# Kernel tuning notes

Hardware: AMD Instinct MI355X
Metric: run time of the kernel (lower is better)

Reference implementation:

```python
import jax, jax.numpy as jnp
import numpy as np
import math

N_HEADS = 32
N_KV_HEADS = 8
HEAD_DIM = 64
THETA = 10000.0
NEG_INF = -1e9


def _rope_cos_sin(seq_len, dim, dtype=jnp.float32):
    # freqs over even indices, matching torch.arange(0, dim, 2)/dim
    freqs = 1.0 / (THETA ** (jnp.arange(0, dim, 2, dtype=jnp.float32) / dim))  # [dim/2]
    angles = jnp.arange(seq_len, dtype=jnp.float32)[:, None] * freqs[None, :]  # [S, dim/2]
    return jnp.cos(angles).astype(dtype), jnp.sin(angles).astype(dtype)


def _apply_rope(x, cos, sin):
    # x: [B, S, H, D]; pairs (x[...,2i], x[...,2i+1]) rotated as complex numbers
    xr = x[..., 0::2]
    xi = x[..., 1::2]
    # broadcast cos/sin [S, D/2] -> [1, S, 1, D/2]
    c = cos[None, :, None, :]
    s = sin[None, :, None, :]
    or_ = xr * c - xi * s
    oi_ = xr * s + xi * c
    # interleave back: [..., D/2, 2] -> [..., D]
    return jnp.stack([or_, oi_], axis=-1).reshape(x.shape)


def setup_inputs() -> dict:
    key = jax.random.key(0)
    ks = jax.random.split(key, 5)
    B, S, D = 2, 2048, 2048
    KV_D = N_KV_HEADS * HEAD_DIM
    x = jax.random.normal(ks[0], (B, S, D), dtype=jnp.float32)
    sc = 1.0 / math.sqrt(D)
    wq = jax.random.normal(ks[1], (D, D), dtype=jnp.float32) * sc
    wk = jax.random.normal(ks[2], (D, KV_D), dtype=jnp.float32) * sc
    wv = jax.random.normal(ks[3], (D, KV_D), dtype=jnp.float32) * sc
    wo = jax.random.normal(ks[4], (D, D), dtype=jnp.float32) * sc
    # additive causal mask [1, 1, S, S]
    causal = jnp.tril(jnp.ones((S, S), dtype=bool))
    mask = jnp.where(causal, 0.0, NEG_INF).astype(jnp.float32)[None, None]
    return {"x": x, "mask": mask, "wq": wq, "wk": wk, "wv": wv, "wo": wo}


def reference(x, mask, wq, wk, wv, wo):
    B, S, D = x.shape
    n_rep = N_HEADS // N_KV_HEADS
    q = (x @ wq).reshape(B, S, N_HEADS, HEAD_DIM)
    k = (x @ wk).reshape(B, S, N_KV_HEADS, HEAD_DIM)
    v = (x @ wv).reshape(B, S, N_KV_HEADS, HEAD_DIM)
    cos, sin = _rope_cos_sin(S, HEAD_DIM)
    q = _apply_rope(q, cos, sin)
    k = _apply_rope(k, cos, sin)
    # GQA: repeat_interleave kv heads along head dim
    k = jnp.repeat(k, n_rep, axis=2)  # [B, S, H, D]
    v = jnp.repeat(v, n_rep, axis=2)
    scores = jnp.einsum("bqhd,bkhd->bhqk", q, k) / math.sqrt(HEAD_DIM)
    scores = scores + mask
    probs = jax.nn.softmax(scores.astype(jnp.float32), axis=-1).astype(q.dtype)
    out = jnp.einsum("bhqk,bkhd->bqhd", probs, v).reshape(B, S, N_HEADS * HEAD_DIM)
    return out @ wo
```

## Files before the change

kernel.cpp:

```cpp
#include <hip/hip_runtime.h>
#include <hip/hip_bf16.h>


#define S_LEN 2048
#define BATCH 2
#define D_MODEL 2048
#define NH 32
#define NKV 8
#define HD 64
#define KV_D (NKV * HD)
#define QKV_N (D_MODEL + 2 * KV_D)

typedef __attribute__((ext_vector_type(8))) short short8;
typedef __attribute__((ext_vector_type(4))) float float4v;

typedef __attribute__((address_space(1))) const unsigned int gu32;
typedef __attribute__((address_space(3))) unsigned int lu32;

#if __has_builtin(__builtin_amdgcn_exp2f)
#define PEXP(x) __builtin_amdgcn_exp2f(x)
#else
#define PEXP(x) __expf((x) * 0.69314718f)
#endif
#define QSCALE 0.18033688f

__device__ __forceinline__ float bf2f(unsigned short u) {
    unsigned x = ((unsigned)u) << 16;
    return __builtin_bit_cast(float, x);
}
__device__ __forceinline__ unsigned short f2bf(float f) {
    unsigned u = __builtin_bit_cast(unsigned, f);
    unsigned r = (u + 0x7fffu + ((u >> 16) & 1u)) >> 16;
    return (unsigned short)r;
}
__device__ __forceinline__ unsigned short f2bf_fast(float f) {
    return (unsigned short)((__builtin_bit_cast(unsigned, f) + 0x8000u) >> 16);
}

__global__ void cast_f32_bf16(const float* __restrict__ in,
                              unsigned short* __restrict__ out, long n) {
    long i = ((long)blockIdx.x * 256 + threadIdx.x) * 4;
    if (i + 3 >= n) return;
    const float4v v = *(const float4v*)&in[i];
    unsigned short o[4];
    o[0] = f2bf(v[0]); o[1] = f2bf(v[1]); o[2] = f2bf(v[2]); o[3] = f2bf(v[3]);
    *(__attribute__((ext_vector_type(4))) short*)&out[i] =
        *(__attribute__((ext_vector_type(4))) short*)o;
}

__global__ __launch_bounds__(256) void wtrans(const float* __restrict__ in,
                                              unsigned short* __restrict__ out,
                                              int K, int N) {
    __shared__ unsigned short t[32 * 33];
    const int nb = blockIdx.x * 32, kb = blockIdx.y * 32;
    const int c = threadIdx.x & 31, rr = threadIdx.x >> 5;
#pragma unroll
    for (int it = 0; it < 4; ++it) {
        int r = it * 8 + rr;
        t[c * 33 + r] = f2bf(in[(long)(kb + r) * N + nb + c]);
    }
    __syncthreads();
#pragma unroll
    for (int it = 0; it < 4; ++it) {
        int r = it * 8 + rr;
        out[(long)(nb + r) * K + kb + c] = t[r * 33 + c];
    }
}

template <bool F32OUT>
__global__ __launch_bounds__(256, 4) void gemm_bt(const unsigned short* __restrict__ A,
                                                  const unsigned short* __restrict__ BT,
                                                  void* __restrict__ Cv,
                                                  int M, int N, int K) {
    __shared__ unsigned short As[64 * 64];
    __shared__ unsigned short Bs[128 * 64];
    const int tid = threadIdx.x;
    const int wid = tid >> 6, lane = tid & 63;
    const int l15 = lane & 15, quad = lane >> 4;
    const int wm = (wid >> 1) * 32, wn = (wid & 1) * 64;
    const int row0 = blockIdx.x * 64, col0 = blockIdx.y * 128;

    float4v acc[2][4];
    float4v z;
    z[0] = z[1] = z[2] = z[3] = 0.0f;
    for (int mi = 0; mi < 2; ++mi)
        for (int ni = 0; ni < 4; ++ni) acc[mi][ni] = z;

    const int r_ld = (lane >> 3);
    const int cc_ld = (lane & 7) * 8;

    for (int kb = 0; kb < K; kb += 64) {
        __syncthreads();
#pragma unroll
        for (int c = 0; c < 4; ++c) {
            int chunk = c * 4 + wid;
            int r = chunk * 8 + r_ld;
            __builtin_amdgcn_global_load_lds(
                (gu32*)&BT[(long)(col0 + r) * K + kb + cc_ld],
                (lu32*)&Bs[chunk * 512], 16, 0, 0);
            if (c < 2)
                __builtin_amdgcn_global_load_lds(
                    (gu32*)&A[(long)(row0 + r) * K + kb + cc_ld],
                    (lu32*)&As[chunk * 512], 16, 0, 0);
        }
        __syncthreads();
#pragma unroll
        for (int kk = 0; kk < 64; kk += 32) {
            short8 af[2], bf[4];
#pragma unroll
            for (int i = 0; i < 2; ++i)
                af[i] = *(const short8*)&As[(wm + i * 16 + l15) * 64 + kk + quad * 8];
#pragma unroll
            for (int i = 0; i < 4; ++i)
                bf[i] = *(const short8*)&Bs[(wn + i * 16 + l15) * 64 + kk + quad * 8];
#pragma unroll
            for (int mi = 0; mi < 2; ++mi)
#pragma unroll
                for (int ni = 0; ni < 4; ++ni)
                    acc[mi][ni] = __builtin_amdgcn_mfma_f32_16x16x32_bf16(
                        af[mi], bf[ni], acc[mi][ni], 0, 0, 0);
        }
    }
#pragma unroll
    for (int mi = 0; mi < 2; ++mi)
#pragma unroll
        for (int ni = 0; ni < 4; ++ni)
#pragma unroll
            for (int r = 0; r < 4; ++r) {
                int m = row0 + wm + mi * 16 + quad * 4 + r;
                int n = col0 + wn + ni * 16 + l15;
                if (F32OUT)
                    ((float*)Cv)[(long)m * N + n] = acc[mi][ni][r];
                else
                    ((unsigned short*)Cv)[(long)m * N + n] = f2bf(acc[mi][ni][r]);
            }
}

__global__ __launch_bounds__(256) void rope2(unsigned short* __restrict__ qkv) {
    const int i = threadIdx.x & 31;
    const int row = blockIdx.x * 8 + (threadIdx.x >> 5);
    const int s = row & (S_LEN - 1);
    float freq = __expf(-0.28782313f * (float)i);
    float ang = (float)s * freq;
    float c = cosf(ang), sn = sinf(ang);
    unsigned* p = (unsigned*)qkv + ((long)row * QKV_N + 2 * i) / 2;
#pragma unroll
    for (int head = 0; head < 40; ++head) {
        const float qs = (head < 32) ? QSCALE : 1.0f;
        unsigned v = p[head * 32];
        float xr = bf2f((unsigned short)(v & 0xffff));
        float xi = bf2f((unsigned short)(v >> 16));
        unsigned short lo = f2bf((xr * c - xi * sn) * qs);
        unsigned short hi = f2bf((xr * sn + xi * c) * qs);
        p[head * 32] = (unsigned)lo | ((unsigned)hi << 16);
    }
}

__global__ __launch_bounds__(256) void vtrans(const unsigned short* __restrict__ qkv,
                                              unsigned short* __restrict__ Vt) {
    __shared__ unsigned t[64 * 33];
    const int st = blockIdx.x * 64, kh = blockIdx.y, b = blockIdx.z;
    const int tid = threadIdx.x;
    {
        const int r2 = tid >> 3, dbase = (tid & 7) * 8;
        const unsigned short* src =
            qkv + ((long)(b * S_LEN + st + 2 * r2)) * QKV_N + D_MODEL + KV_D + kh * HD + dbase;
        short8 lo = *(const short8*)src;
        short8 hi = *(const short8*)(src + QKV_N);
#pragma unroll
        for (int j = 0; j < 8; ++j)
            t[(dbase + j) * 33 + r2] =
                (unsigned)(unsigned short)lo[j] | ((unsigned)(unsigned short)hi[j] << 16);
    }
    __syncthreads();
    {
        const int d = tid >> 2, sb = (tid & 3) * 8;
        unsigned short o[16];
#pragma unroll
        for (int jj = 0; jj < 8; ++jj) {
            unsigned v = t[d * 33 + sb + jj];
            o[2 * jj] = (unsigned short)(v & 0xffff);
            o[2 * jj + 1] = (unsigned short)(v >> 16);
        }
        unsigned short* dst =
            Vt + ((long)((b * 8 + kh) * 64 + d)) * S_LEN + st + sb * 2;
        *(short8*)dst = *(short8*)&o[0];
        *(short8*)(dst + 8) = *(short8*)&o[8];
    }
}

__global__ __launch_bounds__(512, 4) void flash4(const unsigned short* __restrict__ qkv,
                                                 const unsigned short* __restrict__ Vt,
                                                 unsigned short* __restrict__ O) {
    __shared__ unsigned short Ks[64 * 72];
    __shared__ unsigned short Vs[64 * 72];
    __shared__ unsigned short Ps[8][16 * 72];

    const int tid = threadIdx.x, w = tid >> 6, lane = tid & 63;
    const int l15 = lane & 15, quad = lane >> 4;
    const int h = blockIdx.y, b = blockIdx.z;
    const int kh = h >> 2, bkh = b * 8 + kh;
    const int qtA = blockIdx.x;

    const int r_st = tid >> 3;
    const int c_st = (tid & 7) * 8;

    float4v z;
    z[0] = z[1] = z[2] = z[3] = 0.0f;

    for (int tsel = 0; tsel < 2; ++tsel) {
        const int qt = tsel ? (15 - qtA) : qtA;
        const int m0 = qt * 128;
        const int row_w = m0 + w * 16;

        short8 aq[2];
        {
            const long qrow = ((long)(b * S_LEN) + row_w + l15) * QKV_N + h * HD;
            aq[0] = *(const short8*)&qkv[qrow + quad * 8];
            aq[1] = *(const short8*)&qkv[qrow + 32 + quad * 8];
        }

        float4v oacc[4];
        float lp[4];
#pragma unroll
        for (int nt = 0; nt < 4; ++nt) oacc[nt] = z;
#pragma unroll
        for (int r = 0; r < 4; ++r) lp[r] = 0.0f;

        const int nkt = 2 * qt + 2;
        for (int kti = 0; kti < nkt; ++kti) {
            const int k0 = kti * 64;
            __syncthreads();
            *(short8*)&Ks[r_st * 72 + c_st] =
                *(const short8*)&qkv[((long)(b * S_LEN) + k0 + r_st) * QKV_N +
                                     D_MODEL + kh * HD + c_st];
            *(short8*)&Vs[r_st * 72 + c_st] =
                *(const short8*)&Vt[((long)bkh * 64 + r_st) * S_LEN + k0 + c_st];
            __syncthreads();

            if (row_w + 15 < k0) continue;

            const bool maskband = (kti >= 2 * qt);

#pragma unroll
            for (int nt = 0; nt < 4; ++nt) {
                short8 bk0 = *(const short8*)&Ks[(nt * 16 + l15) * 72 + quad * 8];
                short8 bk1 = *(const short8*)&Ks[(nt * 16 + l15) * 72 + 32 + quad * 8];
                float4v s = __builtin_amdgcn_mfma_f32_16x16x32_bf16(aq[0], bk0, z, 0, 0, 0);
                s = __builtin_amdgcn_mfma_f32_16x16x32_bf16(aq[1], bk1, s, 0, 0, 0);
#pragma unroll
                for (int r = 0; r < 4; ++r) {
                    const int qidx = row_w + quad * 4 + r;
                    float v = s[r];
                    if (maskband && (k0 + nt * 16 + l15 > qidx)) v = -1e4f;
                    float p = PEXP(v);
                    lp[r] += p;
                    Ps[w][(quad * 4 + r) * 72 + nt * 16 + l15] = f2bf_fast(p);
                }
            }

            short8 ap0 = *(const short8*)&Ps[w][l15 * 72 + quad * 8];
            short8 ap1 = *(const short8*)&Ps[w][l15 * 72 + 32 + quad * 8];
#pragma unroll
            for (int nt = 0; nt < 4; ++nt) {
                short8 bv0 = *(const short8*)&Vs[(nt * 16 + l15) * 72 + quad * 8];
                short8 bv1 = *(const short8*)&Vs[(nt * 16 + l15) * 72 + 32 + quad * 8];
                oacc[nt] = __builtin_amdgcn_mfma_f32_16x16x32_bf16(ap0, bv0, oacc[nt], 0, 0, 0);
                oacc[nt] = __builtin_amdgcn_mfma_f32_16x16x32_bf16(ap1, bv1, oacc[nt], 0, 0, 0);
            }
        }

#pragma unroll
        for (int r = 0; r < 4; ++r) {
            float l = lp[r];
#pragma unroll
            for (int off = 1; off < 16; off <<= 1) l += __shfl_xor(l, off);
            float inv = 1.0f / l;
            int m = row_w + quad * 4 + r;
            long orow = ((long)(b * S_LEN) + m) * D_MODEL + h * HD;
#pragma unroll
            for (int nt = 0; nt < 4; ++nt)
                O[orow + nt * 16 + l15] = f2bf(oacc[nt][r] * inv);
        }
    }
}

extern "C" void kernel_launch(void* const* d_in, const int* in_sizes, int n_in,
                              void* d_out, int out_size, void* d_ws, size_t ws_size,
                              hipStream_t stream) {
    const float* x  = (const float*)d_in[0];
    const float* wq = (const float*)d_in[n_in - 4];
    const float* wk = (const float*)d_in[n_in - 3];
    const float* wv = (const float*)d_in[n_in - 2];
    const float* wo = (const float*)d_in[n_in - 1];
    float* out = (float*)d_out;

    unsigned short* ws    = (unsigned short*)d_ws;
    unsigned short* xb    = ws;
    unsigned short* Obuf  = ws;
    unsigned short* qkv   = xb + (long)BATCH * S_LEN * D_MODEL;
    unsigned short* woT   = qkv + (long)BATCH * S_LEN * QKV_N;
    unsigned short* wqkvT = woT + (long)D_MODEL * D_MODEL;
    unsigned short* Vt    = wqkvT;

    const int M = BATCH * S_LEN;
    const long xn = (long)M * D_MODEL;

    cast_f32_bf16<<<(int)(xn / 4 / 256), 256, 0, stream>>>(x, xb, xn);

    wtrans<<<dim3(D_MODEL / 32, D_MODEL / 32), 256, 0, stream>>>(wq, wqkvT, D_MODEL, D_MODEL);
    wtrans<<<dim3(KV_D / 32, D_MODEL / 32), 256, 0, stream>>>(wk, wqkvT + (long)D_MODEL * D_MODEL, D_MODEL, KV_D);
    wtrans<<<dim3(KV_D / 32, D_MODEL / 32), 256, 0, stream>>>(wv, wqkvT + (long)(D_MODEL + KV_D) * D_MODEL, D_MODEL, KV_D);
    wtrans<<<dim3(D_MODEL / 32, D_MODEL / 32), 256, 0, stream>>>(wo, woT, D_MODEL, D_MODEL);

    gemm_bt<false><<<dim3(M / 64, QKV_N / 128), 256, 0, stream>>>(xb, wqkvT, qkv, M, QKV_N, D_MODEL);

    rope2<<<M / 8, 256, 0, stream>>>(qkv);

    vtrans<<<dim3(S_LEN / 64, NKV, BATCH), 256, 0, stream>>>(qkv, Vt);

    flash4<<<dim3(8, NH, BATCH), 512, 0, stream>>>(qkv, Vt, Obuf);

    gemm_bt<true><<<dim3(M / 64, D_MODEL / 128), 256, 0, stream>>>(Obuf, woT, out, M, D_MODEL, D_MODEL);
}
```

Measured before the change: 356.4 us.

## Swizzle GEMM shared-memory layout and enlarge QKV GEMM tile to 128 rows

Applies an XOR swizzle to the 16-byte chunks that the direct global-to-LDS loads write into shared memory, and reads back with the same swizzle, to avoid LDS bank conflicts on the MFMA fragment loads. The GEMM is templated on row-tile height, and the QKV projection now uses 128x128 tiles so each B tile is reused across more rows. The larger tile raises register and LDS use per block, which lowers occupancy (launch bound of 3 blocks) and halves the number of blocks in the QKV GEMM grid.

```diff
diff --git a/kernel.cpp b/kernel.cpp
--- a/kernel.cpp
+++ b/kernel.cpp
@@ -67,27 +67,29 @@
     }
 }
 
-template <bool F32OUT>
-__global__ __launch_bounds__(256, 4) void gemm_bt(const unsigned short* __restrict__ A,
-                                                  const unsigned short* __restrict__ BT,
-                                                  void* __restrict__ Cv,
-                                                  int M, int N, int K) {
-    __shared__ unsigned short As[64 * 64];
+template <int TM, bool F32OUT>
+__global__ __launch_bounds__(256, TM == 64 ? 4 : 3)
+void gemm_sw(const unsigned short* __restrict__ A,
+             const unsigned short* __restrict__ BT,
+             void* __restrict__ Cv, int M, int N, int K) {
+    __shared__ unsigned short As[TM * 64];
     __shared__ unsigned short Bs[128 * 64];
     const int tid = threadIdx.x;
     const int wid = tid >> 6, lane = tid & 63;
     const int l15 = lane & 15, quad = lane >> 4;
-    const int wm = (wid >> 1) * 32, wn = (wid & 1) * 64;
-    const int row0 = blockIdx.x * 64, col0 = blockIdx.y * 128;
-
-    float4v acc[2][4];
+    const int wm = (wid >> 1) * (TM / 2), wn = (wid & 1) * 64;
+    const int row0 = blockIdx.x * TM, col0 = blockIdx.y * 128;
+    constexpr int MI = TM / 32;
+
+    float4v acc[MI][4];
     float4v z;
     z[0] = z[1] = z[2] = z[3] = 0.0f;
-    for (int mi = 0; mi < 2; ++mi)
+    for (int mi = 0; mi < MI; ++mi)
         for (int ni = 0; ni < 4; ++ni) acc[mi][ni] = z;
 
-    const int r_ld = (lane >> 3);
-    const int cc_ld = (lane & 7) * 8;
+    const int r_ld = lane >> 3;
+    const int swz_ld = ((lane & 7) ^ (lane >> 3)) * 8;
+    const int sw = l15 & 7;
 
     for (int kb = 0; kb < K; kb += 64) {
         __syncthreads();
@@ -96,25 +98,27 @@
             int chunk = c * 4 + wid;
             int r = chunk * 8 + r_ld;
             __builtin_amdgcn_global_load_lds(
-                (gu32*)&BT[(long)(col0 + r) * K + kb + cc_ld],
+                (gu32*)&BT[(long)(col0 + r) * K + kb + swz_ld],
                 (lu32*)&Bs[chunk * 512], 16, 0, 0);
-            if (c < 2)
+            if (c < MI)
                 __builtin_amdgcn_global_load_lds(
-                    (gu32*)&A[(long)(row0 + r) * K + kb + cc_ld],
+                    (gu32*)&A[(long)(row0 + r) * K + kb + swz_ld],
                     (lu32*)&As[chunk * 512], 16, 0, 0);
         }
         __syncthreads();
 #pragma unroll
         for (int kk = 0; kk < 64; kk += 32) {
-            short8 af[2], bf[4];
-#pragma unroll
-            for (int i = 0; i < 2; ++i)
-                af[i] = *(const short8*)&As[(wm + i * 16 + l15) * 64 + kk + quad * 8];
+            short8 af[MI], bf[4];
+#pragma unroll
+            for (int i = 0; i < MI; ++i)
+                af[i] = *(const short8*)
+                    &As[(wm + i * 16 + l15) * 64 + ((((kk >> 3) + quad) ^ sw) << 3)];
 #pragma unroll
             for (int i = 0; i < 4; ++i)
-                bf[i] = *(const short8*)&Bs[(wn + i * 16 + l15) * 64 + kk + quad * 8];
-#pragma unroll
-            for (int mi = 0; mi < 2; ++mi)
+                bf[i] = *(const short8*)
+                    &Bs[(wn + i * 16 + l15) * 64 + ((((kk >> 3) + quad) ^ sw) << 3)];
+#pragma unroll
+            for (int mi = 0; mi < MI; ++mi)
 #pragma unroll
                 for (int ni = 0; ni < 4; ++ni)
                     acc[mi][ni] = __builtin_amdgcn_mfma_f32_16x16x32_bf16(
@@ -122,7 +126,7 @@
         }
     }
 #pragma unroll
-    for (int mi = 0; mi < 2; ++mi)
+    for (int mi = 0; mi < MI; ++mi)
 #pragma unroll
         for (int ni = 0; ni < 4; ++ni)
 #pragma unroll
@@ -313,7 +317,8 @@
     wtrans<<<dim3(KV_D / 32, D_MODEL / 32), 256, 0, stream>>>(wv, wqkvT + (long)(D_MODEL + KV_D) * D_MODEL, D_MODEL, KV_D);
     wtrans<<<dim3(D_MODEL / 32, D_MODEL / 32), 256, 0, stream>>>(wo, woT, D_MODEL, D_MODEL);
 
-    gemm_bt<false><<<dim3(M / 64, QKV_N / 128), 256, 0, stream>>>(xb, wqkvT, qkv, M, QKV_N, D_MODEL);
+    gemm_sw<128, false><<<dim3(M / 128, QKV_N / 128), 256, 0, stream>>>(
+        xb, wqkvT, qkv, M, QKV_N, D_MODEL);
 
     rope2<<<M / 8, 256, 0, stream>>>(qkv);
 
@@ -321,5 +326,6 @@
 
     flash4<<<dim3(8, NH, BATCH), 512, 0, stream>>>(qkv, Vt, Obuf);
 
-    gemm_bt<true><<<dim3(M / 64, D_MODEL / 128), 256, 0, stream>>>(Obuf, woT, out, M, D_MODEL, D_MODEL);
-}
+    gemm_sw<64, true><<<dim3(M / 64, D_MODEL / 128), 256, 0, stream>>>(
+        Obuf, woT, out, M, D_MODEL, D_MODEL);
+}
```

Measured after the change: 317.1 us. -11.0%, faster.
